# Kernel tuning notes

Hardware: AMD Instinct MI355X
Metric: run time of the kernel (lower is better)

## Reference

```python
import jax, jax.numpy as jnp
import numpy as np

B, S, D = 4, 1024, 1024
H = 16
HD = D // H  # 64
NPOS = 64


def setup_inputs() -> dict:
    key = jax.random.key(0)
    ks = jax.random.split(key, 12)
    f = lambda k, shape, s=0.02: jax.random.normal(k, shape, dtype=jnp.float32) * s
    return {
        "q": jax.random.normal(ks[0], (B, S, D), dtype=jnp.float32),
        "k": jax.random.normal(ks[1], (B, S, D), dtype=jnp.float32),
        "v": jax.random.normal(ks[2], (B, S, D), dtype=jnp.float32),
        "Wq_w": f(ks[3], (D, D)), "Wq_b": f(ks[4], (D,)),
        "Wk_w": f(ks[5], (D, D)), "Wk_b": f(ks[6], (D,)),
        "Wv_w": f(ks[7], (D, D)), "Wv_b": f(ks[8], (D,)),
        "Wo_w": f(ks[9], (D, D)), "Wo_b": f(ks[10], (D,)),
        "pos_emb": f(ks[11], (HD, NPOS)),  # torch param is [1,1,head_dim,npos_max]
    }


def _proj(x, w, b):
    # nn.Linear: x @ w.T + b, then split heads -> [B, H, S, HD]
    y = jnp.einsum("bsd,ed->bse", x, w) + b
    bsz, s, _ = y.shape
    return y.reshape(bsz, s, H, HD).transpose(0, 2, 1, 3)


def reference(q, k, v, Wq_w, Wq_b, Wk_w, Wk_b, Wv_w, Wv_b, Wo_w, Wo_b, pos_emb):
    Q = _proj(q, Wq_w, Wq_b)
    K = _proj(k, Wk_w, Wk_b)
    V = _proj(v, Wv_w, Wv_b)

    scale = 1.0 / np.sqrt(HD).astype(np.float32)
    logits = jnp.einsum("bhqd,bhkd->bhqk", Q, K) * scale  # [B,H,S,S]

    # CoPE: sigmoid gates -> reverse cumsum -> interpolated position-logit gather
    gates = jax.nn.sigmoid(logits)
    pos = jnp.flip(jnp.cumsum(jnp.flip(gates, axis=-1), axis=-1), axis=-1)
    pos = jnp.minimum(pos, NPOS - 1)
    pos_floor = jnp.floor(pos)
    pos_ceil = jnp.ceil(pos)
    logits_int = jnp.einsum("bhqd,dn->bhqn", Q, pos_emb)  # [B,H,S,NPOS]
    lc = jnp.take_along_axis(logits_int, pos_ceil.astype(jnp.int32), axis=-1)
    lf = jnp.take_along_axis(logits_int, pos_floor.astype(jnp.int32), axis=-1)
    w = pos - pos_floor
    logits = logits + lc * w + lf * (1.0 - w)

    score = jax.nn.softmax(logits, axis=-1)
    out = jnp.einsum("bhqk,bhkd->bhqd", score, V)
    out = out.transpose(0, 2, 1, 3).reshape(q.shape[0], q.shape[1], D)
    return jnp.einsum("bsd,ed->bse", out, Wo_w) + Wo_b
```

## Files before the change

kernel.cpp:

```cpp
#include <hip/hip_runtime.h>
#include <hip/hip_bf16.h>

typedef __attribute__((ext_vector_type(8))) short short8;
typedef __attribute__((ext_vector_type(4))) float f32x4;
typedef unsigned short us;

#define MFMA16(a,b,c) __builtin_amdgcn_mfma_f32_16x16x32_bf16((a),(b),(c),0,0,0)
#define LOG2E 1.4426950408889634f

static __device__ __forceinline__ us bf16r(float x){
  unsigned u = __builtin_bit_cast(unsigned, x);
  u = u + 0x7fffu + ((u >> 16) & 1u);
  return (us)(u >> 16);
}
static __device__ __forceinline__ unsigned cvtpk(float a, float b){
  unsigned r; asm("v_cvt_pk_bf16_f32 %0, %1, %2" : "=v"(r) : "v"(a), "v"(b)); return r;
}
static __device__ __forceinline__ short8 cvt8(float4 a, float4 b){
  uint4 u; u.x = cvtpk(a.x, a.y); u.y = cvtpk(a.z, a.w);
  u.z = cvtpk(b.x, b.y); u.w = cvtpk(b.z, b.w);
  return __builtin_bit_cast(short8, u);
}
static __device__ __forceinline__ float b2f(us h){
  return __builtin_bit_cast(float, (unsigned)h << 16);
}
static __device__ __forceinline__ float exp2fast(float x){
  float r; asm("v_exp_f32 %0, %1" : "=v"(r) : "v"(x)); return r;
}
static __device__ __forceinline__ float rcpfast(float x){
  float r; asm("v_rcp_f32 %0, %1" : "=v"(r) : "v"(x)); return r;
}
static __device__ __forceinline__ float fractfast(float x){
  float r; asm("v_fract_f32 %0, %1" : "=v"(r) : "v"(x)); return r;
}

__global__ __launch_bounds__(256)
void transpose_pe(const float* __restrict__ pe, us* __restrict__ peT){
  const int t = threadIdx.x;
  const int n = t & 63, dq = t >> 6;
#pragma unroll
  for (int j = 0; j < 16; ++j){
    const int d = dq * 16 + j;
    peT[n * 64 + d] = bf16r(pe[d * 64 + n] * LOG2E);
  }
}

__global__ __launch_bounds__(256)
void transpose_v(const us* __restrict__ Vb, us* __restrict__ VT){
  __shared__ __align__(16) us tile[64 * 72];
  const int t = threadIdx.x;
  const int stile = blockIdx.x & 15;
  const int bh = blockIdx.x >> 4;
  const int b = bh >> 4, h = bh & 15;
  const int s0 = stile << 6;
#pragma unroll
  for (int c = 0; c < 2; ++c){
    const int idx = t + (c << 8);
    const int sr = idx >> 3, cw = idx & 7;
    *(short8*)&tile[sr * 72 + cw * 8] =
        *(const short8*)(Vb + ((size_t)(b * 1024 + s0 + sr)) * 1024 + h * 64 + cw * 8);
  }
  __syncthreads();
#pragma unroll
  for (int c = 0; c < 2; ++c){
    const int idx = t + (c << 8);
    const int dr = idx >> 3, sw = idx & 7;
    short8 o;
#pragma unroll
    for (int j = 0; j < 8; ++j) o[j] = (short)tile[(sw * 8 + j) * 72 + dr];
    *(short8*)(VT + ((size_t)(bh * 64 + dr)) * 1024 + s0 + sw * 8) = o;
  }
}

template<bool A_BF16, bool OUT_BF16>
__global__ __launch_bounds__(256)
void gemm3(const void* __restrict__ Av0, const void* __restrict__ Av1, const void* __restrict__ Av2,
           const float* __restrict__ W0, const float* __restrict__ W1, const float* __restrict__ W2,
           const float* __restrict__ bp0, const float* __restrict__ bp1, const float* __restrict__ bp2,
           void* __restrict__ O0, void* __restrict__ O1, void* __restrict__ O2){
  __shared__ __align__(16) us Al[128 * 64];
  __shared__ __align__(16) us Bl[128 * 64];
  const int sel = blockIdx.y;
  const void* Av   = sel == 0 ? Av0 : (sel == 1 ? Av1 : Av2);
  const float* Wm  = sel == 0 ? W0  : (sel == 1 ? W1  : W2);
  const float* bias = sel == 0 ? bp0 : (sel == 1 ? bp1 : bp2);
  void* Ov         = sel == 0 ? O0  : (sel == 1 ? O1  : O2);
  const int tid = threadIdx.x;
  const int bm = blockIdx.x & 31, bn = blockIdx.x >> 5;
  const int m0 = bm << 7, n0 = bn << 7;
  const int w = tid >> 6, l = tid & 63;
  const int lr = l & 15, lg = l >> 4;
  const int wm = (w & 1) << 6, wn = (w >> 1) << 6;
  int srow[4], scol[4], sdst[4];
#pragma unroll
  for (int c = 0; c < 4; ++c){
    const int idx = tid + (c << 8);
    const int r = idx >> 3, cw = idx & 7;
    srow[c] = r; scol[c] = cw << 3;
    sdst[c] = r * 64 + ((cw << 3) ^ ((r & 7) << 3));
  }
  const int swz = (lr & 7) << 3;
  f32x4 acc[4][4];
#pragma unroll
  for (int i = 0; i < 4; ++i)
#pragma unroll
    for (int j = 0; j < 4; ++j) acc[i][j] = (f32x4){0.f, 0.f, 0.f, 0.f};

  auto ldA = [&](int c, int k) -> short8 {
    if constexpr (A_BF16){
      return *(const short8*)((const us*)Av + (size_t)(m0 + srow[c]) * 1024 + k + scol[c]);
    } else {
      const float* p = (const float*)Av + (size_t)(m0 + srow[c]) * 1024 + k + scol[c];
      return cvt8(*(const float4*)p, *(const float4*)(p + 4));
    }
  };
  auto ldW = [&](int c, int k) -> short8 {
    const float* p = Wm + (size_t)(n0 + srow[c]) * 1024 + k + scol[c];
    return cvt8(*(const float4*)p, *(const float4*)(p + 4));
  };

  short8 av[4], bv[4];
#pragma unroll
  for (int c = 0; c < 4; ++c){ av[c] = ldA(c, 0); bv[c] = ldW(c, 0); }

  for (int k0 = 0; k0 < 1024; k0 += 64){
    __syncthreads();
#pragma unroll
    for (int c = 0; c < 4; ++c){
      *(short8*)&Al[sdst[c]] = av[c];
      *(short8*)&Bl[sdst[c]] = bv[c];
    }
    __syncthreads();
    if (k0 < 960){
#pragma unroll
      for (int c = 0; c < 4; ++c){ av[c] = ldA(c, k0 + 64); bv[c] = ldW(c, k0 + 64); }
    }
#pragma unroll
    for (int ks = 0; ks < 2; ++ks){
      short8 af[4], bfv[4];
#pragma unroll
      for (int mt = 0; mt < 4; ++mt)
        af[mt] = *(const short8*)&Al[(wm + mt * 16 + lr) * 64 + (((ks << 5) + (lg << 3)) ^ swz)];
#pragma unroll
      for (int nt = 0; nt < 4; ++nt)
        bfv[nt] = *(const short8*)&Bl[(wn + nt * 16 + lr) * 64 + (((ks << 5) + (lg << 3)) ^ swz)];
#pragma unroll
      for (int mt = 0; mt < 4; ++mt)
#pragma unroll
        for (int nt = 0; nt < 4; ++nt)
          acc[mt][nt] = MFMA16(af[mt], bfv[nt], acc[mt][nt]);
    }
  }
  float bb[4];
#pragma unroll
  for (int nt = 0; nt < 4; ++nt) bb[nt] = bias[n0 + wn + nt * 16 + lr];
#pragma unroll
  for (int mt = 0; mt < 4; ++mt)
#pragma unroll
    for (int nt = 0; nt < 4; ++nt)
#pragma unroll
      for (int r = 0; r < 4; ++r){
        const size_t m = m0 + wm + mt * 16 + lg * 4 + r;
        const size_t n = n0 + wn + nt * 16 + lr;
        const float vv = acc[mt][nt][r] + bb[nt];
        if (OUT_BF16) ((us*)Ov)[m * 1024 + n] = bf16r(vv);
        else          ((float*)Ov)[m * 1024 + n] = vv;
      }
}

__global__ __launch_bounds__(256, 4)
void cope_attn_v9(const us* __restrict__ Qb, const us* __restrict__ Kb,
                  const us* __restrict__ VT, const us* __restrict__ peT,
                  us* __restrict__ Ob){
  __shared__ __align__(16) us yl[16 * 512];
  __shared__ float sums[16];
  const int tid = threadIdx.x;
  const int w = tid >> 6, l = tid & 63;
  const int lr = l & 15, lg = l >> 4;
  const int qt = blockIdx.x & 63;
  const int bh = blockIdx.x >> 6;
  const int b = bh >> 4, h = bh & 15;
  const int q0 = qt << 4;
  const us* Qh = Qb + ((size_t)(b * 1024 + q0)) * 1024 + h * 64;
  const us* Kh = Kb + ((size_t)(b * 1024)) * 1024 + h * 64;
  const us* Vh = VT + ((size_t)bh) * 64 * 1024;
  const float QSC = 0.125f * LOG2E;

  const short8 aq0 = *(const short8*)(Qh + (size_t)lr * 1024 + lg * 8);
  const short8 aq1 = *(const short8*)(Qh + (size_t)lr * 1024 + 32 + lg * 8);

  {
    f32x4 a = (f32x4){0.f, 0.f, 0.f, 0.f};
    const short8 p0 = *(const short8*)(peT + (size_t)(w * 16 + lr) * 64 + lg * 8);
    const short8 p1 = *(const short8*)(peT + (size_t)(w * 16 + lr) * 64 + 32 + lg * 8);
    a = MFMA16(aq0, p0, a);
    a = MFMA16(aq1, p1, a);
#pragma unroll
    for (int r = 0; r < 4; ++r) yl[(lg * 4 + r) * 64 + w * 16 + lr] = bf16r(a[r]);
  }
  __syncthreads();
  unsigned trow[4];
#pragma unroll
  for (int rr = 0; rr < 4; ++rr){
    const int row = w * 4 + rr;
    const us lov = yl[row * 64 + l];
    const us hiv = (l < 63) ? yl[row * 64 + l + 1] : lov;
    const float dif = b2f(hiv) - b2f(lov);
    trow[rr] = (unsigned)lov | ((unsigned)bf16r(dif) << 16);
  }

  float carry[4] = {0.f, 0.f, 0.f, 0.f};
  f32x4 oacc = (f32x4){0.f, 0.f, 0.f, 0.f};
  const int d0 = w * 16;
  const int psw = lr & 7;

  for (int c = 1; c >= 0; --c){
    const int koff = c << 9;
    __syncthreads();
    {
      const int kbase = w << 7;
      const us* Kw = Kh + (size_t)(koff + kbase + lr) * 1024 + lg * 8;
      for (int t = 0; t < 8; ++t){
        const short8 b0 = *(const short8*)(Kw + (size_t)(t * 16) * 1024);
        const short8 b1 = *(const short8*)(Kw + (size_t)(t * 16) * 1024 + 32);
        f32x4 a = (f32x4){0.f, 0.f, 0.f, 0.f};
        a = MFMA16(aq0, b0, a);
        a = MFMA16(aq1, b1, a);
        const int kc = kbase + t * 16 + lr;
        const unsigned p01 = cvtpk(a[0] * QSC, a[1] * QSC);
        const unsigned p23 = cvtpk(a[2] * QSC, a[3] * QSC);
        const int r0 = lg * 4;
        yl[(r0 + 0) * 512 + (((kc >> 3) ^ ((r0 + 0) & 7)) << 3) + (kc & 7)] = (us)p01;
        yl[(r0 + 1) * 512 + (((kc >> 3) ^ ((r0 + 1) & 7)) << 3) + (kc & 7)] = (us)(p01 >> 16);
        yl[(r0 + 2) * 512 + (((kc >> 3) ^ ((r0 + 2) & 7)) << 3) + (kc & 7)] = (us)p23;
        yl[(r0 + 3) * 512 + (((kc >> 3) ^ ((r0 + 3) & 7)) << 3) + (kc & 7)] = (us)(p23 >> 16);
      }
    }
    __syncthreads();
#pragma unroll
    for (int rr = 0; rr < 4; ++rr){
      const int row = w * 4 + rr;
      const int ad = row * 512 + ((l ^ (row & 7)) << 3);
      const short8 y0 = *(const short8*)&yl[ad];
      float x[8];
#pragma unroll
      for (int j = 0; j < 8; ++j) x[j] = b2f((us)y0[j]);
      float pref[8];
      float s = 0.f;
#pragma unroll
      for (int i = 0; i < 8; ++i){
        const float g = rcpfast(1.f + exp2fast(-x[i]));
        pref[i] = s;
        s += g;
      }
      float run = s;
#pragma unroll
      for (int off = 1; off < 64; off <<= 1){
        const float t2 = __shfl_up(run, off);
        if (l >= off) run += t2;
      }
      const float T = __shfl(run, 63);
      const float base = carry[rr] + T - (run - s);
      carry[rr] += T;
      const unsigned tbl = trow[rr];
      float sum = 0.f;
#pragma unroll
      for (int i = 0; i < 8; ++i){
        float p = base - pref[i];
        p = __builtin_amdgcn_fmed3f(p, 0.f, 63.f);
        const int il = (int)p;
        const float wt = fractfast(p);
        const unsigned pr = (unsigned)__builtin_amdgcn_ds_bpermute(il << 2, (int)tbl);
        const float lo  = __builtin_bit_cast(float, pr << 16);
        const float dif = __builtin_bit_cast(float, pr & 0xffff0000u);
        const float e = exp2fast(x[i] + lo + wt * dif);
        x[i] = e;
        sum += e;
      }
#pragma unroll
      for (int off = 1; off < 64; off <<= 1) sum += __shfl_xor(sum, off);
      if (l == 0){
        if (c == 1) sums[row] = sum;
        else        sums[row] += sum;
      }
      uint4 ua;
      ua.x = cvtpk(x[0], x[1]); ua.y = cvtpk(x[2], x[3]);
      ua.z = cvtpk(x[4], x[5]); ua.w = cvtpk(x[6], x[7]);
      *(uint4*)&yl[ad] = ua;
    }
    __syncthreads();
    {
      const us* Vw = Vh + (size_t)(d0 + lr) * 1024 + koff + lg * 8;
      for (int ks = 0; ks < 16; ++ks){
        const short8 vb = *(const short8*)(Vw + ks * 32);
        const short8 pa = *(const short8*)&yl[lr * 512 + ((((ks << 2) + lg) ^ psw) << 3)];
        oacc = MFMA16(pa, vb, oacc);
      }
    }
  }
  __syncthreads();
#pragma unroll
  for (int r = 0; r < 4; ++r){
    const float inv = rcpfast(sums[lg * 4 + r]);
    Ob[((size_t)(b * 1024 + q0 + lg * 4 + r)) * 1024 + h * 64 + d0 + lr] = bf16r(oacc[r] * inv);
  }
}

extern "C" void kernel_launch(void* const* d_in, const int* in_sizes, int n_in,
                              void* d_out, int out_size, void* d_ws, size_t ws_size,
                              hipStream_t stream) {
  const float* q    = (const float*)d_in[0];
  const float* k    = (const float*)d_in[1];
  const float* v    = (const float*)d_in[2];
  const float* Wq_w = (const float*)d_in[3];
  const float* Wq_b = (const float*)d_in[4];
  const float* Wk_w = (const float*)d_in[5];
  const float* Wk_b = (const float*)d_in[6];
  const float* Wv_w = (const float*)d_in[7];
  const float* Wv_b = (const float*)d_in[8];
  const float* Wo_w = (const float*)d_in[9];
  const float* Wo_b = (const float*)d_in[10];
  const float* pe   = (const float*)d_in[11];
  float* out = (float*)d_out;

  char* W = (char*)d_ws;
  const size_t MB = (size_t)1 << 20;
  us* Qbf = (us*)(W);
  us* Kbf = (us*)(W + 8 * MB);
  us* Vbf = (us*)(W + 16 * MB);
  us* VTb = (us*)(W + 24 * MB);
  us* Obf = (us*)(W + 32 * MB);
  us* peT = (us*)(W + 40 * MB);

  transpose_pe<<<1, 256, 0, stream>>>(pe, peT);
  gemm3<false, true><<<dim3(256, 3), 256, 0, stream>>>(
      q, k, v, Wq_w, Wk_w, Wv_w, Wq_b, Wk_b, Wv_b, Qbf, Kbf, Vbf);
  transpose_v<<<1024, 256, 0, stream>>>(Vbf, VTb);
  cope_attn_v9<<<4096, 256, 0, stream>>>(Qbf, Kbf, VTb, peT, Obf);
  gemm3<true, false><<<dim3(256, 1), 256, 0, stream>>>(
      Obf, Obf, Obf, Wo_w, Wo_w, Wo_w, Wo_b, Wo_b, Wo_b, out, out, out);
}
```

Measured before the change: 231.0 us.

## Restructure CoPE attention to keep scores in registers with split-K per wave

Rewrites the attention kernel so each wave computes transposed score tiles (K as A operand) and keeps logits and gates packed in registers, instead of staging the full 16x512 score block through shared memory. Cumulative gate sums use cross-lane xor shuffles plus a small shared per-wave total rather than a 64-step shfl_up scan. The position-table lookup now reads from shared memory. For the second key chunk, if every row's carry already saturates at 63, a shortcut path skips the sigmoid and gather work. P·V runs split-K across waves via bpermute-repacked fragments, with a shared-memory reduction of partial outputs at the end. It also swizzles the block order for L2 locality. The trade-off is higher register pressure, since the launch bound no longer requests 4 blocks, and an extra final reduction through shared memory.

```diff
diff --git a/kernel.cpp b/kernel.cpp
--- a/kernel.cpp
+++ b/kernel.cpp
@@ -24,6 +24,12 @@
 static __device__ __forceinline__ float b2f(us h){
   return __builtin_bit_cast(float, (unsigned)h << 16);
 }
+static __device__ __forceinline__ float PKLO(unsigned u){
+  return __builtin_bit_cast(float, u << 16);
+}
+static __device__ __forceinline__ float PKHI(unsigned u){
+  return __builtin_bit_cast(float, u & 0xffff0000u);
+}
 static __device__ __forceinline__ float exp2fast(float x){
   float r; asm("v_exp_f32 %0, %1" : "=v"(r) : "v"(x)); return r;
 }
@@ -32,6 +38,15 @@
 }
 static __device__ __forceinline__ float fractfast(float x){
   float r; asm("v_fract_f32 %0, %1" : "=v"(r) : "v"(x)); return r;
+}
+static __device__ __forceinline__ float sigm(float y){
+  return rcpfast(1.f + exp2fast(-y));
+}
+static __device__ __forceinline__ unsigned bperm(int lanebyte, unsigned v){
+  return (unsigned)__builtin_amdgcn_ds_bpermute(lanebyte, (int)v);
+}
+static __device__ __forceinline__ float sxor(float v, int m){
+  return __shfl_xor(v, m);
 }
 
 __global__ __launch_bounds__(256)
@@ -168,141 +183,212 @@
       }
 }
 
-__global__ __launch_bounds__(256, 4)
-void cope_attn_v9(const us* __restrict__ Qb, const us* __restrict__ Kb,
-                  const us* __restrict__ VT, const us* __restrict__ peT,
-                  us* __restrict__ Ob){
-  __shared__ __align__(16) us yl[16 * 512];
-  __shared__ float sums[16];
+__global__ __launch_bounds__(256)
+void cope_attn_v14(const us* __restrict__ Qb, const us* __restrict__ Kb,
+                   const us* __restrict__ VT, const us* __restrict__ peT,
+                   us* __restrict__ Ob){
+  __shared__ __align__(16) char smem[21248];
+  unsigned* pkt  = (unsigned*)smem;
+  us*      li16  = (us*)(smem + 4096);
+  float*   opart = (float*)(smem + 4096);
+  float*   wtot  = (float*)(smem + 20480);
+  float*   dsumL = (float*)(smem + 20992);
+
   const int tid = threadIdx.x;
   const int w = tid >> 6, l = tid & 63;
   const int lr = l & 15, lg = l >> 4;
-  const int qt = blockIdx.x & 63;
-  const int bh = blockIdx.x >> 6;
+  const int wg = ((blockIdx.x & 7) << 9) | (blockIdx.x >> 3);
+  const int qt = wg & 63;
+  const int bh = wg >> 6;
   const int b = bh >> 4, h = bh & 15;
   const int q0 = qt << 4;
   const us* Qh = Qb + ((size_t)(b * 1024 + q0)) * 1024 + h * 64;
   const us* Kh = Kb + ((size_t)(b * 1024)) * 1024 + h * 64;
   const us* Vh = VT + ((size_t)bh) * 64 * 1024;
   const float QSC = 0.125f * LOG2E;
-
-  const short8 aq0 = *(const short8*)(Qh + (size_t)lr * 1024 + lg * 8);
-  const short8 aq1 = *(const short8*)(Qh + (size_t)lr * 1024 + 32 + lg * 8);
+  const f32x4 zf = (f32x4){0.f, 0.f, 0.f, 0.f};
+
+  const short8 bq0 = *(const short8*)(Qh + (size_t)lr * 1024 + lg * 8);
+  const short8 bq1 = *(const short8*)(Qh + (size_t)lr * 1024 + 32 + lg * 8);
 
   {
-    f32x4 a = (f32x4){0.f, 0.f, 0.f, 0.f};
+    f32x4 a = zf;
     const short8 p0 = *(const short8*)(peT + (size_t)(w * 16 + lr) * 64 + lg * 8);
     const short8 p1 = *(const short8*)(peT + (size_t)(w * 16 + lr) * 64 + 32 + lg * 8);
-    a = MFMA16(aq0, p0, a);
-    a = MFMA16(aq1, p1, a);
-#pragma unroll
-    for (int r = 0; r < 4; ++r) yl[(lg * 4 + r) * 64 + w * 16 + lr] = bf16r(a[r]);
+    a = MFMA16(bq0, p0, a);
+    a = MFMA16(bq1, p1, a);
+#pragma unroll
+    for (int r = 0; r < 4; ++r) li16[(lg * 4 + r) * 64 + w * 16 + lr] = bf16r(a[r]);
   }
   __syncthreads();
-  unsigned trow[4];
-#pragma unroll
-  for (int rr = 0; rr < 4; ++rr){
-    const int row = w * 4 + rr;
-    const us lov = yl[row * 64 + l];
-    const us hiv = (l < 63) ? yl[row * 64 + l + 1] : lov;
-    const float dif = b2f(hiv) - b2f(lov);
-    trow[rr] = (unsigned)lov | ((unsigned)bf16r(dif) << 16);
-  }
-
-  float carry[4] = {0.f, 0.f, 0.f, 0.f};
-  f32x4 oacc = (f32x4){0.f, 0.f, 0.f, 0.f};
-  const int d0 = w * 16;
-  const int psw = lr & 7;
-
+  unsigned myPk[4];
+#pragma unroll
+  for (int i = 0; i < 4; ++i){
+    const int e = tid * 4 + i;
+    const int qq = e >> 6, n = e & 63;
+    const us lov = li16[qq * 64 + n];
+    const us hiv = (n < 63) ? li16[qq * 64 + n + 1] : lov;
+    myPk[i] = (unsigned)lov | ((unsigned)bf16r(b2f(hiv) - b2f(lov)) << 16);
+  }
+  __syncthreads();
+#pragma unroll
+  for (int i = 0; i < 4; ++i) pkt[tid * 4 + i] = myPk[i];
+  __syncthreads();
+  const unsigned* pq = pkt + (lr << 6);
+  const float li63q = PKLO(pq[63]);
+
+  f32x4 oacc[4];
+#pragma unroll
+  for (int dt = 0; dt < 4; ++dt) oacc[dt] = zf;
+  float esum = 0.f;
+  float carryq = 0.f;
+  bool clamp0 = false;
+
+#pragma unroll
   for (int c = 1; c >= 0; --c){
-    const int koff = c << 9;
-    __syncthreads();
-    {
-      const int kbase = w << 7;
-      const us* Kw = Kh + (size_t)(koff + kbase + lr) * 1024 + lg * 8;
+    const int kwbase = (c << 9) + (w << 7);
+    unsigned ypk[8][2], gpk[8][2];
+#pragma unroll
+    for (int t = 0; t < 8; ++t){
+      const us* Kp = Kh + (size_t)(kwbase + t * 16 + lr) * 1024 + lg * 8;
+      const short8 a0 = *(const short8*)Kp;
+      const short8 a1 = *(const short8*)(Kp + 32);
+      f32x4 s = zf;
+      s = MFMA16(a0, bq0, s);
+      s = MFMA16(a1, bq1, s);
+      ypk[t][0] = cvtpk(s[0] * QSC, s[1] * QSC);
+      ypk[t][1] = cvtpk(s[2] * QSC, s[3] * QSC);
+    }
+    const bool fullpath = (c == 1) || (!clamp0);
+    if (fullpath){
+      float ltot = 0.f;
+#pragma unroll
       for (int t = 0; t < 8; ++t){
-        const short8 b0 = *(const short8*)(Kw + (size_t)(t * 16) * 1024);
-        const short8 b1 = *(const short8*)(Kw + (size_t)(t * 16) * 1024 + 32);
-        f32x4 a = (f32x4){0.f, 0.f, 0.f, 0.f};
-        a = MFMA16(aq0, b0, a);
-        a = MFMA16(aq1, b1, a);
-        const int kc = kbase + t * 16 + lr;
-        const unsigned p01 = cvtpk(a[0] * QSC, a[1] * QSC);
-        const unsigned p23 = cvtpk(a[2] * QSC, a[3] * QSC);
-        const int r0 = lg * 4;
-        yl[(r0 + 0) * 512 + (((kc >> 3) ^ ((r0 + 0) & 7)) << 3) + (kc & 7)] = (us)p01;
-        yl[(r0 + 1) * 512 + (((kc >> 3) ^ ((r0 + 1) & 7)) << 3) + (kc & 7)] = (us)(p01 >> 16);
-        yl[(r0 + 2) * 512 + (((kc >> 3) ^ ((r0 + 2) & 7)) << 3) + (kc & 7)] = (us)p23;
-        yl[(r0 + 3) * 512 + (((kc >> 3) ^ ((r0 + 3) & 7)) << 3) + (kc & 7)] = (us)(p23 >> 16);
-      }
-    }
-    __syncthreads();
-#pragma unroll
-    for (int rr = 0; rr < 4; ++rr){
-      const int row = w * 4 + rr;
-      const int ad = row * 512 + ((l ^ (row & 7)) << 3);
-      const short8 y0 = *(const short8*)&yl[ad];
-      float x[8];
-#pragma unroll
-      for (int j = 0; j < 8; ++j) x[j] = b2f((us)y0[j]);
-      float pref[8];
-      float s = 0.f;
-#pragma unroll
-      for (int i = 0; i < 8; ++i){
-        const float g = rcpfast(1.f + exp2fast(-x[i]));
-        pref[i] = s;
-        s += g;
-      }
-      float run = s;
-#pragma unroll
-      for (int off = 1; off < 64; off <<= 1){
-        const float t2 = __shfl_up(run, off);
-        if (l >= off) run += t2;
-      }
-      const float T = __shfl(run, 63);
-      const float base = carry[rr] + T - (run - s);
-      carry[rr] += T;
-      const unsigned tbl = trow[rr];
-      float sum = 0.f;
-#pragma unroll
-      for (int i = 0; i < 8; ++i){
-        float p = base - pref[i];
-        p = __builtin_amdgcn_fmed3f(p, 0.f, 63.f);
-        const int il = (int)p;
-        const float wt = fractfast(p);
-        const unsigned pr = (unsigned)__builtin_amdgcn_ds_bpermute(il << 2, (int)tbl);
-        const float lo  = __builtin_bit_cast(float, pr << 16);
-        const float dif = __builtin_bit_cast(float, pr & 0xffff0000u);
-        const float e = exp2fast(x[i] + lo + wt * dif);
-        x[i] = e;
-        sum += e;
-      }
-#pragma unroll
-      for (int off = 1; off < 64; off <<= 1) sum += __shfl_xor(sum, off);
-      if (l == 0){
-        if (c == 1) sums[row] = sum;
-        else        sums[row] += sum;
-      }
-      uint4 ua;
-      ua.x = cvtpk(x[0], x[1]); ua.y = cvtpk(x[2], x[3]);
-      ua.z = cvtpk(x[4], x[5]); ua.w = cvtpk(x[6], x[7]);
-      *(uint4*)&yl[ad] = ua;
-    }
-    __syncthreads();
-    {
-      const us* Vw = Vh + (size_t)(d0 + lr) * 1024 + koff + lg * 8;
-      for (int ks = 0; ks < 16; ++ks){
-        const short8 vb = *(const short8*)(Vw + ks * 32);
-        const short8 pa = *(const short8*)&yl[lr * 512 + ((((ks << 2) + lg) ^ psw) << 3)];
-        oacc = MFMA16(pa, vb, oacc);
-      }
-    }
-  }
+        const float g0 = sigm(PKLO(ypk[t][0])), g1 = sigm(PKHI(ypk[t][0]));
+        const float g2 = sigm(PKLO(ypk[t][1])), g3 = sigm(PKHI(ypk[t][1]));
+        gpk[t][0] = cvtpk(g0, g1); gpk[t][1] = cvtpk(g2, g3);
+        ltot += (g0 + g1) + (g2 + g3);
+      }
+      float t1 = ltot + sxor(ltot, 16);
+      const float Twq = t1 + sxor(t1, 32);
+      if (l < 16) wtot[c * 64 + w * 16 + l] = Twq;
+      __syncthreads();
+      const float tw0 = wtot[c * 64 + 0 + lr];
+      const float tw1 = wtot[c * 64 + 16 + lr];
+      const float tw2 = wtot[c * 64 + 32 + lr];
+      const float tw3 = wtot[c * 64 + 48 + lr];
+      float shw = 0.f;
+      if (w == 0) shw = tw1 + tw2 + tw3;
+      else if (w == 1) shw = tw2 + tw3;
+      else if (w == 2) shw = tw3;
+      const float carry_in = shw + (c == 0 ? carryq : 0.f);
+      if (c == 1){
+        carryq = (tw0 + tw1) + (tw2 + tw3);
+        clamp0 = __all(carryq >= 63.f);
+      }
+      float sT[8], sufg[8], tsuf[8];
+#pragma unroll
+      for (int t = 0; t < 8; ++t){
+        const float g0 = PKLO(gpk[t][0]), g1 = PKHI(gpk[t][0]);
+        const float g2 = PKLO(gpk[t][1]), g3 = PKHI(gpk[t][1]);
+        const float st = (g0 + g1) + (g2 + g3);
+        const float sa = sxor(st, 16);
+        const float sb = sxor(st, 32);
+        const float sc = sxor(sa, 32);
+        sT[t] = st;
+        sufg[t] = (lg == 0) ? (sa + sb + sc) : (lg == 1) ? (sb + sc) : (lg == 2) ? sa : 0.f;
+        tsuf[t] = st + sa + sb + sc;
+      }
+      float run = 0.f;
+#pragma unroll
+      for (int t = 7; t >= 0; --t){ const float tmp = tsuf[t]; tsuf[t] = run; run += tmp; }
+#pragma unroll
+      for (int t = 0; t < 8; ++t){
+        const float g0 = PKLO(gpk[t][0]), g1 = PKHI(gpk[t][0]);
+        const float g2 = PKLO(gpk[t][1]);
+        const float y0 = PKLO(ypk[t][0]), y1 = PKHI(ypk[t][0]);
+        const float y2 = PKLO(ypk[t][1]), y3 = PKHI(ypk[t][1]);
+        const float bbv = carry_in + tsuf[t] + sufg[t] + sT[t];
+        float e0, e1, e2, e3;
+        {
+          const float p = __builtin_amdgcn_fmed3f(bbv, 0.f, 63.f);
+          const unsigned pr = pq[(int)p];
+          e0 = exp2fast(y0 + PKLO(pr) + fractfast(p) * PKHI(pr));
+        }
+        {
+          const float p = __builtin_amdgcn_fmed3f(bbv - g0, 0.f, 63.f);
+          const unsigned pr = pq[(int)p];
+          e1 = exp2fast(y1 + PKLO(pr) + fractfast(p) * PKHI(pr));
+        }
+        {
+          const float p = __builtin_amdgcn_fmed3f(bbv - (g0 + g1), 0.f, 63.f);
+          const unsigned pr = pq[(int)p];
+          e2 = exp2fast(y2 + PKLO(pr) + fractfast(p) * PKHI(pr));
+        }
+        {
+          const float p = __builtin_amdgcn_fmed3f(bbv - ((g0 + g1) + g2), 0.f, 63.f);
+          const unsigned pr = pq[(int)p];
+          e3 = exp2fast(y3 + PKLO(pr) + fractfast(p) * PKHI(pr));
+        }
+        esum += (e0 + e1) + (e2 + e3);
+        gpk[t][0] = cvtpk(e0, e1); gpk[t][1] = cvtpk(e2, e3);
+      }
+    } else {
+#pragma unroll
+      for (int t = 0; t < 8; ++t){
+        const float e0 = exp2fast(PKLO(ypk[t][0]) + li63q);
+        const float e1 = exp2fast(PKHI(ypk[t][0]) + li63q);
+        const float e2 = exp2fast(PKLO(ypk[t][1]) + li63q);
+        const float e3 = exp2fast(PKHI(ypk[t][1]) + li63q);
+        esum += (e0 + e1) + (e2 + e3);
+        gpk[t][0] = cvtpk(e0, e1); gpk[t][1] = cvtpk(e2, e3);
+      }
+    }
+    const int sa4 = (lr + ((lg & 1) << 5)) << 2;
+    const int sb4 = sa4 + 64;
+    const bool hi2 = ((lg >> 1) & 1) != 0;
+#pragma unroll
+    for (int u = 0; u < 4; ++u){
+      const unsigned p0a = bperm(sa4, gpk[2 * u][0]),     p0b = bperm(sa4, gpk[2 * u + 1][0]);
+      const unsigned p1a = bperm(sa4, gpk[2 * u][1]),     p1b = bperm(sa4, gpk[2 * u + 1][1]);
+      const unsigned p2a = bperm(sb4, gpk[2 * u][0]),     p2b = bperm(sb4, gpk[2 * u + 1][0]);
+      const unsigned p3a = bperm(sb4, gpk[2 * u][1]),     p3b = bperm(sb4, gpk[2 * u + 1][1]);
+      uint4 af;
+      af.x = hi2 ? p0b : p0a;
+      af.y = hi2 ? p1b : p1a;
+      af.z = hi2 ? p2b : p2a;
+      af.w = hi2 ? p3b : p3a;
+      const short8 pa = __builtin_bit_cast(short8, af);
+#pragma unroll
+      for (int dt = 0; dt < 4; ++dt){
+        const short8 vb = *(const short8*)(Vh + (size_t)(dt * 16 + lr) * 1024 + kwbase + u * 32 + lg * 8);
+        oacc[dt] = MFMA16(pa, vb, oacc[dt]);
+      }
+    }
+  }
+  float d1 = esum + sxor(esum, 16);
+  const float dq = d1 + sxor(d1, 32);
+  if (l < 16) dsumL[w * 16 + l] = dq;
+#pragma unroll
+  for (int dt = 0; dt < 4; ++dt)
+#pragma unroll
+    for (int r = 0; r < 4; ++r)
+      opart[w * 1024 + (lg * 4 + r) * 64 + dt * 16 + lr] = oacc[dt][r];
   __syncthreads();
-#pragma unroll
-  for (int r = 0; r < 4; ++r){
-    const float inv = rcpfast(sums[lg * 4 + r]);
-    Ob[((size_t)(b * 1024 + q0 + lg * 4 + r)) * 1024 + h * 64 + d0 + lr] = bf16r(oacc[r] * inv);
+  {
+    const int qq = tid >> 4;
+    const int d0 = (tid & 15) << 2;
+    const float inv = rcpfast(dsumL[qq] + dsumL[16 + qq] + dsumL[32 + qq] + dsumL[48 + qq]);
+    float o[4];
+#pragma unroll
+    for (int i = 0; i < 4; ++i){
+      const int off = qq * 64 + d0 + i;
+      o[i] = ((opart[off] + opart[1024 + off]) + (opart[2048 + off] + opart[3072 + off])) * inv;
+    }
+    uint2 pk2o;
+    pk2o.x = cvtpk(o[0], o[1]);
+    pk2o.y = cvtpk(o[2], o[3]);
+    *(uint2*)&Ob[((size_t)(b * 1024 + q0 + qq)) * 1024 + h * 64 + d0] = pk2o;
   }
 }
 
@@ -336,7 +422,7 @@
   gemm3<false, true><<<dim3(256, 3), 256, 0, stream>>>(
       q, k, v, Wq_w, Wk_w, Wv_w, Wq_b, Wk_b, Wv_b, Qbf, Kbf, Vbf);
   transpose_v<<<1024, 256, 0, stream>>>(Vbf, VTb);
-  cope_attn_v9<<<4096, 256, 0, stream>>>(Qbf, Kbf, VTb, peT, Obf);
+  cope_attn_v14<<<4096, 256, 0, stream>>>(Qbf, Kbf, VTb, peT, Obf);
   gemm3<true, false><<<dim3(256, 1), 256, 0, stream>>>(
       Obf, Obf, Obf, Wo_w, Wo_w, Wo_w, Wo_b, Wo_b, Wo_b, out, out, out);
 }
```

After: 221.2 us. 1.04x faster.
